# Kernel tuning notes

Hardware: AMD Instinct MI355X
Metric: run time of the kernel (lower is better)

Reference implementation:

```python
import jax, jax.numpy as jnp
import numpy as np

N_HIDDEN = 2048
N_HEADS = 64
EXPAND = 2
D_STATE = 128
D_CONV = 4
CHUNK = 128
DT_MIN = 0.001
DT_MAX = 0.1
INNER = EXPAND * N_HIDDEN            # 4096
HEAD_DIM = INNER // N_HEADS          # 64
CONV_DIM = INNER + 2 * D_STATE       # 4352
D_IN_PROJ = 2 * INNER + 2 * D_STATE + N_HEADS  # 8512
EPS = 1e-6


def setup_inputs() -> dict:
    key = jax.random.key(0)
    ks = jax.random.split(key, 10)
    B, L = 2, 2048
    s = lambda fan_in: 1.0 / np.sqrt(fan_in)
    return {
        "x": jax.random.normal(ks[0], (B, L, N_HIDDEN), jnp.float32),
        "W_in": jax.random.normal(ks[1], (N_HIDDEN, D_IN_PROJ), jnp.float32) * s(N_HIDDEN),
        "b_in": jnp.zeros((D_IN_PROJ,), jnp.float32),
        "conv_w": jax.random.normal(ks[2], (D_CONV, 1, CONV_DIM), jnp.float32) * s(D_CONV),
        "conv_b": jnp.zeros((CONV_DIM,), jnp.float32),
        "A_log": jnp.log(jnp.arange(1, N_HEADS + 1, dtype=jnp.float32)),
        "dt_bias": jax.random.normal(ks[3], (N_HEADS,), jnp.float32) * 0.1,
        "D_param": jnp.ones((N_HEADS,), jnp.float32),
        "norm_w": jnp.ones((INNER,), jnp.float32),
        "W_out": jax.random.normal(ks[4], (INNER, N_HIDDEN), jnp.float32) * s(INNER),
        "b_out": jnp.zeros((N_HIDDEN,), jnp.float32),
    }


def _segsum(x):
    t = x.shape[-1]
    cs = jnp.cumsum(x, axis=-1)
    seg = cs[..., :, None] - cs[..., None, :]
    mask = jnp.tril(jnp.ones((t, t), dtype=bool))
    return jnp.where(mask, seg, -jnp.inf)


def _ssd(x, dt, a, b_mat, c_mat, d, dt_bias):
    # x: (B,L,H,P)  dt: (B,L,H)  a: (H,)  b_mat/c_mat: (B,L,H,N)  d: (H,)
    bsz, seq, h, p = x.shape
    dt = jnp.clip(jax.nn.softplus(dt + dt_bias), DT_MIN, DT_MAX)
    d_res = d.reshape(1, 1, h, 1) * x
    x_disc = x * dt[..., None]
    a_disc = a * dt                                   # (B,L,H)
    ch = lambda t_: t_.reshape(bsz, seq // CHUNK, CHUNK, *t_.shape[2:])
    x_blk, b_blk, c_blk = ch(x_disc), ch(b_mat), ch(c_mat)
    a_blk = jnp.transpose(ch(a_disc), (0, 3, 1, 2))   # (B,H,C,Lc)
    a_cum = jnp.cumsum(a_blk, axis=-1)
    l_mat = jnp.exp(_segsum(a_blk))                   # (B,H,C,Lc,Lc)
    y_diag = jnp.einsum("bclhn,bcshn,bhcls,bcshp->bclhp", c_blk, b_blk, l_mat, x_blk)
    decay_states = jnp.exp(a_cum[..., -1:] - a_cum)
    states = jnp.einsum("bclhn,bhcl,bclhp->bchpn", b_blk, decay_states, x_blk)
    states = jnp.concatenate([jnp.zeros_like(states[:, :1]), states], axis=1)
    a_end = jnp.pad(a_cum[..., -1], ((0, 0), (0, 0), (1, 0)))
    decay_chunk = jnp.exp(_segsum(a_end))
    new_states = jnp.einsum("bhzc,bchpn->bzhpn", decay_chunk, states)
    states = new_states[:, :-1]
    y_off = jnp.einsum("bclhn,bchpn,bhcl->bclhp", c_blk, states, jnp.exp(a_cum))
    y = (y_diag + y_off).reshape(bsz, seq, h, p)
    return y + d_res


def reference(x, W_in, b_in, conv_w, conv_b, A_log, dt_bias, D_param, norm_w, W_out, b_out):
    B, L, _ = x.shape
    zxbcdt = x @ W_in + b_in
    z = zxbcdt[..., :INNER]
    xBC = zxbcdt[..., INNER:INNER + CONV_DIM]
    dt = zxbcdt[..., -N_HEADS:]
    # causal depthwise conv1d + silu
    xp = jnp.pad(xBC, ((0, 0), (D_CONV - 1, 0), (0, 0)))
    xBC = jax.lax.conv_general_dilated(
        xp, conv_w, window_strides=(1,), padding="VALID",
        dimension_numbers=("NWC", "WIO", "NWC"), feature_group_count=CONV_DIM,
    ) + conv_b
    xBC = jax.nn.silu(xBC)
    x_ssm = xBC[..., :INNER].reshape(B, L, N_HEADS, HEAD_DIM)
    b_mat = jnp.broadcast_to(xBC[..., INNER:INNER + D_STATE][:, :, None, :], (B, L, N_HEADS, D_STATE))
    c_mat = jnp.broadcast_to(xBC[..., INNER + D_STATE:][:, :, None, :], (B, L, N_HEADS, D_STATE))
    a = -jnp.exp(A_log)
    y = _ssd(x_ssm, dt, a, b_mat, c_mat, D_param, dt_bias)
    y = y.reshape(B, L, INNER)
    # gated RMSNorm
    y = y * jax.nn.silu(z)
    y = y * jax.lax.rsqrt(jnp.mean(y * y, axis=-1, keepdims=True) + EPS) * norm_w
    return y @ W_out + b_out
```

## Files before the change

kernel.cpp:

```cpp
#include <hip/hip_runtime.h>
#include <hip/hip_bf16.h>
#include <cstdint>

typedef __bf16 bf16x8 __attribute__((ext_vector_type(8)));
typedef __bf16 bf16x4 __attribute__((ext_vector_type(4)));
typedef float  f4     __attribute__((ext_vector_type(4)));

constexpr int BATCH   = 2;
constexpr int LSEQ    = 2048;
constexpr int NH      = 2048;
constexpr int INNER   = 4096;
constexpr int DSTATE  = 128;
constexpr int CONVD   = 4352;
constexpr int HEADS   = 64;
constexpr int HDIM    = 64;
constexpr int NPROJ   = 8512;
constexpr int NPROJ_P = 8576;
constexpr int NC      = 16;
constexpr int CH      = 128;
constexpr int ROWS    = BATCH * LSEQ;
constexpr int NBC     = BATCH * NC;

__device__ __forceinline__ f4 f4zero() { f4 v; v.x=0.f; v.y=0.f; v.z=0.f; v.w=0.f; return v; }

__device__ __forceinline__ void gload16(const __bf16* g, const char* l) {
    __builtin_amdgcn_global_load_lds((const __attribute__((address_space(1))) void*)g,
                                     (__attribute__((address_space(3))) void*)l, 16, 0, 0);
}

__global__ __launch_bounds__(256) void k_cast_bf16(const float* __restrict__ in,
                                                   __bf16* __restrict__ out, int n4) {
    int i = blockIdx.x * 256 + threadIdx.x;
    if (i >= n4) return;
    f4 v = ((const f4*)in)[i];
    bf16x4 o;
    o[0] = (__bf16)v.x; o[1] = (__bf16)v.y; o[2] = (__bf16)v.z; o[3] = (__bf16)v.w;
    ((bf16x4*)out)[i] = o;
}

__global__ __launch_bounds__(256) void k_transpose_cast(const float* __restrict__ in,
                                                        __bf16* __restrict__ out,
                                                        int R, int C, int Cp) {
    __shared__ float tile[32][33];
    int bn = blockIdx.x * 32, bk = blockIdx.y * 32;
    int tx = threadIdx.x & 31, ty = threadIdx.x >> 5;
#pragma unroll
    for (int i = 0; i < 4; ++i) {
        int k = bk + ty + i * 8, n = bn + tx;
        tile[ty + i * 8][tx] = (k < R && n < C) ? in[(size_t)k * C + n] : 0.f;
    }
    __syncthreads();
#pragma unroll
    for (int i = 0; i < 4; ++i) {
        int n = bn + ty + i * 8, k = bk + tx;
        if (n < Cp && k < R) out[(size_t)n * R + k] = (__bf16)tile[tx][ty + i * 8];
    }
}

template<int EPI>
__global__ __launch_bounds__(256, 2) void k_gemm128(
    const __bf16* __restrict__ A, const __bf16* __restrict__ Bt,
    const float* __restrict__ bias, float* __restrict__ Cf,
    __bf16* __restrict__ zf, __bf16* __restrict__ xbcpre, float* __restrict__ dtraw,
    int N, int K, int gridY) {
    extern __shared__ char smem[];
    constexpr int ABYTES = 128 * 128;
    constexpr int BUFB   = 2 * ABYTES;

    int tid = threadIdx.x, lane = tid & 63, w = tid >> 6;
    int wm = w >> 1, wn = w & 1;

    int bid = blockIdx.x;
    int q = gridDim.x >> 3;
    int wg = (bid & 7) * q + (bid >> 3);
    int bx = wg / gridY, by = wg - bx * gridY;
    int mBase = by * 128, nBase = bx * 128;

    int rl = lane & 15, rq = lane >> 4;
    int kslp = rq ^ (((rl >> 3) & 1) << 1);
    const int rdA = (wm * 64 + rl) * 64 + kslp * 16;
    const int rdB = ABYTES + (wn * 64 + rl) * 64 + kslp * 16;

    int lanep = lane ^ (((lane >> 5) & 1) << 1);
    int srs = lanep >> 2, sksl = lanep & 3;

    const __bf16* sA[4];
    const __bf16* sB[4];
#pragma unroll
    for (int li = 0; li < 4; ++li) {
        sA[li] = A  + (size_t)(mBase + (li & 1) * 64 + w * 16 + srs) * K + (li >> 1) * 32 + sksl * 8;
        sB[li] = Bt + (size_t)(nBase + (li & 1) * 64 + w * 16 + srs) * K + (li >> 1) * 32 + sksl * 8;
    }

    auto stageA = [&](int buf, int li, int kt) {
        gload16(sA[li] + kt, smem + buf * BUFB + (li >> 1) * 8192 + (li & 1) * 4096 + w * 1024);
    };
    auto stageB = [&](int buf, int li, int kt) {
        gload16(sB[li] + kt, smem + buf * BUFB + ABYTES + (li >> 1) * 8192 + (li & 1) * 4096 + w * 1024);
    };

    bf16x8 a0[4], b0[4], a1[4], b1[4];
    auto ldregs = [&](int bufoff, int ks, bf16x8* ar, bf16x8* br) {
#pragma unroll
        for (int i = 0; i < 4; ++i)
            ar[i] = *(const bf16x8*)(smem + bufoff + ks * 8192 + rdA + i * 1024);
#pragma unroll
        for (int i = 0; i < 4; ++i)
            br[i] = *(const bf16x8*)(smem + bufoff + ks * 8192 + rdB + i * 1024);
    };

    f4 acc[4][4];
#pragma unroll
    for (int i = 0; i < 4; ++i)
#pragma unroll
        for (int j = 0; j < 4; ++j) acc[i][j] = f4zero();

    auto domfma = [&](bf16x8* ar, bf16x8* br) {
        __builtin_amdgcn_s_setprio(1);
#pragma unroll
        for (int mi = 0; mi < 4; ++mi)
#pragma unroll
            for (int ni = 0; ni < 4; ++ni)
                acc[mi][ni] = __builtin_amdgcn_mfma_f32_16x16x32_bf16(ar[mi], br[ni], acc[mi][ni], 0, 0, 0);
        __builtin_amdgcn_s_setprio(0);
    };

    const int nt = K >> 6;
#pragma unroll
    for (int li = 0; li < 4; ++li) stageA(0, li, 0);
#pragma unroll
    for (int li = 0; li < 4; ++li) stageB(0, li, 0);
#pragma unroll
    for (int li = 0; li < 4; ++li) stageA(1, li, 64);
    asm volatile("s_waitcnt vmcnt(4)" ::: "memory");
    __builtin_amdgcn_s_barrier();
    ldregs(0, 0, a0, b0);

    for (int t = 0; t < nt; ++t) {
        const int cur = t & 1, bo = cur * BUFB;
        ldregs(bo, 1, a1, b1);
        if (t + 1 < nt) {
            const int ktn = (t + 1) << 6;
#pragma unroll
            for (int li = 0; li < 4; ++li) stageB(cur ^ 1, li, ktn);
        }
        __builtin_amdgcn_sched_barrier(0);
        domfma(a0, b0);
        asm volatile("s_waitcnt lgkmcnt(0)" ::: "memory");
        __builtin_amdgcn_sched_barrier(0);
        __builtin_amdgcn_s_barrier();
        if (t + 2 < nt) {
            const int ktn2 = (t + 2) << 6;
#pragma unroll
            for (int li = 0; li < 4; ++li) stageA(cur, li, ktn2);
        }
        __builtin_amdgcn_sched_barrier(0);
        domfma(a1, b1);
        if (t + 1 < nt) {
            if (t + 2 < nt) {
                asm volatile("s_waitcnt vmcnt(4)" ::: "memory");
            } else {
                asm volatile("s_waitcnt vmcnt(0)" ::: "memory");
            }
            __builtin_amdgcn_s_barrier();
            ldregs((cur ^ 1) * BUFB, 0, a0, b0);
        }
    }

    int cl = lane & 15, rq4 = (lane >> 4) * 4;
#pragma unroll
    for (int nf = 0; nf < 4; ++nf) {
        int col0 = nBase + wn * 64 + nf * 16;
        int col = col0 + cl;
        if constexpr (EPI == 1) {
            if (col0 >= NPROJ) continue;
            float bvv = bias[col];
#pragma unroll
            for (int mf = 0; mf < 4; ++mf) {
#pragma unroll
                for (int j = 0; j < 4; ++j) {
                    int row = mBase + wm * 64 + mf * 16 + rq4 + j;
                    float v = acc[mf][nf][j] + bvv;
                    if (col0 < INNER) {
                        zf[(size_t)row * INNER + col] = (__bf16)v;
                    } else if (col0 < INNER + CONVD) {
                        xbcpre[(size_t)row * CONVD + (col - INNER)] = (__bf16)v;
                    } else {
                        dtraw[(size_t)row * HEADS + (col - INNER - CONVD)] = v;
                    }
                }
            }
        } else {
            float bvv = bias[col];
#pragma unroll
            for (int mf = 0; mf < 4; ++mf)
#pragma unroll
                for (int j = 0; j < 4; ++j) {
                    int row = mBase + wm * 64 + mf * 16 + rq4 + j;
                    Cf[(size_t)row * N + col] = acc[mf][nf][j] + bvv;
                }
        }
    }
}

__global__ __launch_bounds__(256) void k_conv_silu(const __bf16* __restrict__ xbcpre,
                                                   const float* __restrict__ conv_w,
                                                   const float* __restrict__ conv_b,
                                                   __bf16* __restrict__ xbc) {
    int idx = blockIdx.x * 256 + threadIdx.x;
    int c8 = idx % (CONVD / 8);
    int bl = idx / (CONVD / 8);
    int l = bl & (LSEQ - 1);
    int c0 = c8 * 8;
    float acc[8];
    const f4* cb4 = (const f4*)(conv_b + c0);
    f4 b0 = cb4[0], b1 = cb4[1];
#pragma unroll
    for (int k = 0; k < 4; ++k) { acc[k] = b0[k]; acc[k + 4] = b1[k]; }
#pragma unroll
    for (int j = 0; j < 4; ++j) {
        int l2 = l + j - 3;
        if (l2 < 0) continue;
        bf16x8 xv = *(const bf16x8*)(xbcpre + (size_t)(bl + j - 3) * CONVD + c0);
        const f4* w4 = (const f4*)(conv_w + j * CONVD + c0);
        f4 w0 = w4[0], w1 = w4[1];
#pragma unroll
        for (int k = 0; k < 4; ++k) {
            acc[k]     += w0[k] * (float)xv[k];
            acc[k + 4] += w1[k] * (float)xv[k + 4];
        }
    }
    bf16x8 o;
#pragma unroll
    for (int k = 0; k < 8; ++k) {
        float a = acc[k];
        o[k] = (__bf16)(a / (1.f + expf(-a)));
    }
    *(bf16x8*)(xbc + (size_t)bl * CONVD + c0) = o;
}

__global__ __launch_bounds__(256) void k_dt(const float* __restrict__ dtraw,
                                            const float* __restrict__ dt_bias,
                                            float* __restrict__ dtp_t) {
    int idx = blockIdx.x * 256 + threadIdx.x;
    int h = idx & 63;
    int bl = idx >> 6;
    int b = bl >> 11, l = bl & (LSEQ - 1);
    float raw = dtraw[idx] + dt_bias[h];
    float sp = raw > 20.f ? raw : log1pf(expf(raw));
    dtp_t[((size_t)(b * HEADS + h)) * LSEQ + l] = fminf(fmaxf(sp, 0.001f), 0.1f);
}

__global__ __launch_bounds__(256) void k_transpose_bc(const __bf16* __restrict__ xbc,
                                                      __bf16* __restrict__ xT,
                                                      __bf16* __restrict__ BtG) {
    int bid = blockIdx.x;
    int ct = bid % 66;
    int rt = (bid / 66) & 1;
    int bc = bid / 132;
    __shared__ float T[64][65];
    int t = threadIdx.x;
    int lr0 = t >> 3, cg = t & 7;
#pragma unroll
    for (int it = 0; it < 2; ++it) {
        int lr = lr0 + it * 32;
        bf16x8 v = *(const bf16x8*)(xbc + (size_t)(bc * CH + rt * 64 + lr) * CONVD + ct * 64 + cg * 8);
#pragma unroll
        for (int j = 0; j < 8; ++j) T[lr][cg * 8 + j] = (float)v[j];
    }
    __syncthreads();
#pragma unroll
    for (int it = 0; it < 2; ++it) {
        int cl = lr0 + it * 32;
        int c = ct * 64 + cl;
        bf16x8 o;
#pragma unroll
        for (int j = 0; j < 8; ++j) o[j] = (__bf16)T[cg * 8 + j][cl];
        __bf16* dst = (c < INNER)
            ? xT  + ((size_t)bc * INNER + c) * CH + rt * 64 + cg * 8
            : BtG + ((size_t)bc * DSTATE + (c - INNER)) * CH + rt * 64 + cg * 8;
        *(bf16x8*)dst = o;
    }
}

__global__ __launch_bounds__(256) void k_cb(const __bf16* __restrict__ xbc,
                                            float* __restrict__ cbT) {
    int bid = blockIdx.x;
    int lg = bid & 7, bc = bid >> 3;
    int tid = threadIdx.x;
    int e0 = lg * 2048 + tid * 8;
    int l = e0 >> 7;
    int s0 = e0 & 127;
    const __bf16* Crow = xbc + (size_t)(bc * CH + l) * CONVD + INNER + DSTATE;
    const __bf16* B0   = xbc + (size_t)(bc * CH + s0) * CONVD + INNER;
    float acc[8];
#pragma unroll
    for (int j = 0; j < 8; ++j) acc[j] = 0.f;
    for (int n8 = 0; n8 < 16; ++n8) {
        bf16x8 cv = *(const bf16x8*)(Crow + n8 * 8);
        float cf[8];
#pragma unroll
        for (int k = 0; k < 8; ++k) cf[k] = (float)cv[k];
#pragma unroll
        for (int j = 0; j < 8; ++j) {
            bf16x8 bvv = *(const bf16x8*)(B0 + (size_t)j * CONVD + n8 * 8);
#pragma unroll
            for (int k = 0; k < 8; ++k) acc[j] += cf[k] * (float)bvv[k];
        }
    }
    float* dst = cbT + ((size_t)bc << 14) + (l << 7) + s0;
#pragma unroll
    for (int j = 0; j < 8; ++j) dst[j] = (s0 + j <= l) ? acc[j] : 0.f;
}

__global__ __launch_bounds__(256) void k_states(const __bf16* __restrict__ xT,
                                                const __bf16* __restrict__ BtG,
                                                const float* __restrict__ dtp_t,
                                                const float* __restrict__ A_log,
                                                __bf16* __restrict__ states,
                                                float* __restrict__ acum_buf,
                                                float* __restrict__ aend_buf) {
    int bid = blockIdx.x;
    int h = bid & 63, c = (bid >> 6) & 15, b = bid >> 10;
    int bc = b * NC + c, bh = b * HEADS + h;
    int tid = threadIdx.x;
    int lane = tid & 63, w = tid >> 6;
    __shared__ __bf16 Ab[64 * 136];
    __shared__ __bf16 Bb[128 * 136];
    __shared__ float s_ac[128], s_dt[128], s_e[128];
    float a_h = -expf(A_log[h]);

    if (tid < 128) {
        float d = dtp_t[(size_t)bh * LSEQ + c * CH + tid];
        s_dt[tid] = d;
        s_ac[tid] = a_h * d;
    }
    __syncthreads();
    for (int offd = 1; offd < 128; offd <<= 1) {
        float v = 0.f;
        if (tid < 128 && tid >= offd) v = s_ac[tid - offd];
        __syncthreads();
        if (tid < 128) s_ac[tid] += v;
        __syncthreads();
    }
    float aend = s_ac[127];
    if (tid < 128) {
        s_e[tid] = expf(aend - s_ac[tid]) * s_dt[tid];
        acum_buf[((size_t)bh * NC + c) * CH + tid] = s_ac[tid];
    }
    if (tid == 0) aend_buf[bh * NC + c] = aend;
    __syncthreads();

    const __bf16* xrow = xT + ((size_t)bc * INNER + h * HDIM) * CH;
#pragma unroll
    for (int it = 0; it < 4; ++it) {
        int task = it * 256 + tid;
        int p = task >> 4, lg2 = task & 15;
        bf16x8 v = *(const bf16x8*)(xrow + (size_t)p * CH + lg2 * 8);
        bf16x8 o;
#pragma unroll
        for (int j = 0; j < 8; ++j) o[j] = (__bf16)((float)v[j] * s_e[lg2 * 8 + j]);
        *(bf16x8*)&Ab[p * 136 + lg2 * 8] = o;
    }
    const __bf16* brow = BtG + (size_t)bc * DSTATE * CH;
#pragma unroll
    for (int it = 0; it < 8; ++it) {
        int task = it * 256 + tid;
        int n = task >> 4, lg2 = task & 15;
        *(bf16x8*)&Bb[n * 136 + lg2 * 8] = *(const bf16x8*)(brow + (size_t)n * CH + lg2 * 8);
    }
    __syncthreads();

    int rl = lane & 15, kq = (lane >> 4) * 8, rq = lane >> 4;
    f4 acc[8];
#pragma unroll
    for (int i = 0; i < 8; ++i) acc[i] = f4zero();
#pragma unroll
    for (int ks = 0; ks < 4; ++ks) {
        int k0 = ks * 32;
        bf16x8 a = *(const bf16x8*)&Ab[(w * 16 + rl) * 136 + k0 + kq];
#pragma unroll
        for (int nf = 0; nf < 8; ++nf) {
            bf16x8 bfr = *(const bf16x8*)&Bb[(nf * 16 + rl) * 136 + k0 + kq];
            acc[nf] = __builtin_amdgcn_mfma_f32_16x16x32_bf16(a, bfr, acc[nf], 0, 0, 0);
        }
    }
    __syncthreads();
#pragma unroll
    for (int nf = 0; nf < 8; ++nf)
#pragma unroll
        for (int j = 0; j < 4; ++j)
            Ab[(w * 16 + rq * 4 + j) * 136 + nf * 16 + rl] = (__bf16)acc[nf][j];
    __syncthreads();
    __bf16* sbase = states + ((size_t)(bc * HEADS + h)) * (HDIM * DSTATE);
#pragma unroll
    for (int it = 0; it < 4; ++it) {
        int task = it * 256 + tid;
        int p = task >> 4, ng = task & 15;
        *(bf16x8*)(sbase + (size_t)p * DSTATE + ng * 8) = *(const bf16x8*)&Ab[p * 136 + ng * 8];
    }
}

__global__ __launch_bounds__(128) void k_scan(__bf16* __restrict__ states,
                                              const float* __restrict__ aend_buf) {
    int s = blockIdx.x & 7;
    int bh = blockIdx.x >> 3;
    int b = bh >> 6, h = bh & 63;
    int tid = threadIdx.x;
    size_t off = (size_t)s * 1024 + (size_t)tid * 8;
    float run[8];
#pragma unroll
    for (int j = 0; j < 8; ++j) run[j] = 0.f;
    for (int c = 0; c < NC; ++c) {
        float dec = expf(aend_buf[bh * NC + c]);
        __bf16* base = states + ((size_t)((b * NC + c) * HEADS + h)) * (HDIM * DSTATE) + off;
        bf16x8 sv = *(bf16x8*)base;
        bf16x8 o;
#pragma unroll
        for (int j = 0; j < 8; ++j) o[j] = (__bf16)run[j];
        *(bf16x8*)base = o;
#pragma unroll
        for (int j = 0; j < 8; ++j) run[j] = run[j] * dec + (float)sv[j];
    }
}

__global__ __launch_bounds__(256) void k_out(const __bf16* __restrict__ xbc,
                                             const __bf16* __restrict__ xT,
                                             const float* __restrict__ dtp_t,
                                             const float* __restrict__ cbT,
                                             const __bf16* __restrict__ prev,
                                             const float* __restrict__ acum_buf,
                                             const float* __restrict__ D_param,
                                             __bf16* __restrict__ ybuf) {
    int bid = blockIdx.x;
    int h = bid & 63, c = (bid >> 6) & 15, b = bid >> 10;
    int bc = b * NC + c, bh = b * HEADS + h;
    int tid = threadIdx.x;
    int lane = tid & 63, w = tid >> 6;
    __shared__ __bf16 Ab[128 * 136];
    __shared__ __bf16 Bb[64 * 136];
    __shared__ float s_ac[128], s_dt[128];
    if (tid < 128) {
        s_ac[tid] = acum_buf[((size_t)bh * NC + c) * CH + tid];
        s_dt[tid] = dtp_t[(size_t)bh * LSEQ + c * CH + tid];
    }

#pragma unroll
    for (int it = 0; it < 8; ++it) {
        int task = it * 256 + tid;
        int l = task >> 4, ng = task & 15;
        *(bf16x8*)&Ab[l * 136 + ng * 8] =
            *(const bf16x8*)(xbc + (size_t)(bc * CH + l) * CONVD + INNER + DSTATE + ng * 8);
    }
    const __bf16* pbase = prev + ((size_t)(bc * HEADS + h)) * (HDIM * DSTATE);
#pragma unroll
    for (int it = 0; it < 4; ++it) {
        int task = it * 256 + tid;
        int p = task >> 4, ng = task & 15;
        *(bf16x8*)&Bb[p * 136 + ng * 8] = *(const bf16x8*)(pbase + (size_t)p * DSTATE + ng * 8);
    }
    __syncthreads();

    int rl = lane & 15, kq = (lane >> 4) * 8, rq = lane >> 4;
    f4 acc[2][4];
#pragma unroll
    for (int i = 0; i < 2; ++i)
#pragma unroll
        for (int j = 0; j < 4; ++j) acc[i][j] = f4zero();

#pragma unroll
    for (int ks = 0; ks < 4; ++ks) {
        int k0 = ks * 32;
        bf16x8 a0 = *(const bf16x8*)&Ab[(w * 32 + rl) * 136 + k0 + kq];
        bf16x8 a1 = *(const bf16x8*)&Ab[(w * 32 + 16 + rl) * 136 + k0 + kq];
#pragma unroll
        for (int nf = 0; nf < 4; ++nf) {
            bf16x8 bfr = *(const bf16x8*)&Bb[(nf * 16 + rl) * 136 + k0 + kq];
            acc[0][nf] = __builtin_amdgcn_mfma_f32_16x16x32_bf16(a0, bfr, acc[0][nf], 0, 0, 0);
            acc[1][nf] = __builtin_amdgcn_mfma_f32_16x16x32_bf16(a1, bfr, acc[1][nf], 0, 0, 0);
        }
    }
#pragma unroll
    for (int mf = 0; mf < 2; ++mf)
#pragma unroll
        for (int j = 0; j < 4; ++j) {
            float el = expf(s_ac[w * 32 + mf * 16 + rq * 4 + j]);
#pragma unroll
            for (int nf = 0; nf < 4; ++nf) acc[mf][nf][j] *= el;
        }
    __syncthreads();

    const float* cbb = cbT + ((size_t)bc << 14);
#pragma unroll
    for (int it = 0; it < 8; ++it) {
        int task = it * 256 + tid;
        int l = task >> 4, sg = task & 15;
        int s0 = sg * 8;
        const f4* cv4 = (const f4*)(cbb + (l << 7) + s0);
        f4 c0 = cv4[0], c1 = cv4[1];
        float acl = s_ac[l];
        bf16x8 o;
#pragma unroll
        for (int j = 0; j < 8; ++j) {
            int s = s0 + j;
            float cj = (j < 4) ? c0[j] : c1[j - 4];
            float m = 0.f;
            if (s <= l) m = cj * expf(acl - s_ac[s]) * s_dt[s];
            o[j] = (__bf16)m;
        }
        *(bf16x8*)&Ab[l * 136 + s0] = o;
    }
    const __bf16* xrow = xT + ((size_t)bc * INNER + h * HDIM) * CH;
#pragma unroll
    for (int it = 0; it < 4; ++it) {
        int task = it * 256 + tid;
        int p = task >> 4, lg2 = task & 15;
        *(bf16x8*)&Bb[p * 136 + lg2 * 8] = *(const bf16x8*)(xrow + (size_t)p * CH + lg2 * 8);
    }
    __syncthreads();

#pragma unroll
    for (int ks = 0; ks < 4; ++ks) {
        int k0 = ks * 32;
        bf16x8 a0 = *(const bf16x8*)&Ab[(w * 32 + rl) * 136 + k0 + kq];
        bf16x8 a1 = *(const bf16x8*)&Ab[(w * 32 + 16 + rl) * 136 + k0 + kq];
#pragma unroll
        for (int nf = 0; nf < 4; ++nf) {
            bf16x8 bfr = *(const bf16x8*)&Bb[(nf * 16 + rl) * 136 + k0 + kq];
            acc[0][nf] = __builtin_amdgcn_mfma_f32_16x16x32_bf16(a0, bfr, acc[0][nf], 0, 0, 0);
            acc[1][nf] = __builtin_amdgcn_mfma_f32_16x16x32_bf16(a1, bfr, acc[1][nf], 0, 0, 0);
        }
    }
    __syncthreads();

    float* yT = (float*)Ab;
#pragma unroll
    for (int mf = 0; mf < 2; ++mf)
#pragma unroll
        for (int nf = 0; nf < 4; ++nf)
#pragma unroll
            for (int j = 0; j < 4; ++j)
                yT[(w * 32 + mf * 16 + rq * 4 + j) * 68 + nf * 16 + rl] = acc[mf][nf][j];
    __syncthreads();

    float dh = D_param[h];
#pragma unroll
    for (int it = 0; it < 4; ++it) {
        int task = it * 256 + tid;
        int l = task >> 3, pg = task & 7;
        const f4* yv4 = (const f4*)&yT[l * 68 + pg * 8];
        f4 y0 = yv4[0], y1 = yv4[1];
        bf16x8 xv = *(const bf16x8*)(xbc + (size_t)(bc * CH + l) * CONVD + h * HDIM + pg * 8);
        bf16x8 o;
#pragma unroll
        for (int j = 0; j < 4; ++j) {
            o[j]     = (__bf16)(y0[j] + dh * (float)xv[j]);
            o[j + 4] = (__bf16)(y1[j] + dh * (float)xv[j + 4]);
        }
        *(bf16x8*)(ybuf + (size_t)(bc * CH + l) * INNER + h * HDIM + pg * 8) = o;
    }
}

__global__ __launch_bounds__(256) void k_gate_norm(__bf16* __restrict__ ybuf,
                                                   const __bf16* __restrict__ zf,
                                                   const float* __restrict__ norm_w) {
    int row = blockIdx.x, tid = threadIdx.x;
    bf16x8* yrow = (bf16x8*)(ybuf + (size_t)row * INNER);
    const bf16x8* zrow = (const bf16x8*)(zf + (size_t)row * INNER);
    float v[2][8];
    float ss = 0.f;
#pragma unroll
    for (int i = 0; i < 2; ++i) {
        bf16x8 yv = yrow[i * 256 + tid];
        bf16x8 zv = zrow[i * 256 + tid];
#pragma unroll
        for (int j = 0; j < 8; ++j) {
            float z = (float)zv[j];
            float t = (float)yv[j] * (z / (1.f + expf(-z)));
            v[i][j] = t;
            ss += t * t;
        }
    }
#pragma unroll
    for (int off = 32; off > 0; off >>= 1) ss += __shfl_down(ss, off, 64);
    __shared__ float red[4];
    __shared__ float scs;
    if ((tid & 63) == 0) red[tid >> 6] = ss;
    __syncthreads();
    if (tid == 0) scs = rsqrtf((red[0] + red[1] + red[2] + red[3]) * (1.f / INNER) + 1e-6f);
    __syncthreads();
    float scale = scs;
#pragma unroll
    for (int i = 0; i < 2; ++i) {
        const f4* nw = (const f4*)(norm_w + (i * 256 + tid) * 8);
        f4 w0 = nw[0], w1 = nw[1];
        bf16x8 o;
#pragma unroll
        for (int j = 0; j < 4; ++j) {
            o[j]     = (__bf16)(v[i][j]     * scale * w0[j]);
            o[j + 4] = (__bf16)(v[i][j + 4] * scale * w1[j]);
        }
        yrow[i * 256 + tid] = o;
    }
}

extern "C" void kernel_launch(void* const* d_in, const int* in_sizes, int n_in,
                              void* d_out, int out_size, void* d_ws, size_t ws_size,
                              hipStream_t stream) {
    const float* x       = (const float*)d_in[0];
    const float* W_in    = (const float*)d_in[1];
    const float* b_in    = (const float*)d_in[2];
    const float* conv_w  = (const float*)d_in[3];
    const float* conv_b  = (const float*)d_in[4];
    const float* A_log   = (const float*)d_in[5];
    const float* dt_bias = (const float*)d_in[6];
    const float* D_par   = (const float*)d_in[7];
    const float* norm_w  = (const float*)d_in[8];
    const float* W_out   = (const float*)d_in[9];
    const float* b_out   = (const float*)d_in[10];
    float* out = (float*)d_out;

    char* ws = (char*)d_ws;
    constexpr size_t SZ_XBF    = (size_t)ROWS * NH * 2;
    constexpr size_t SZ_WTIN   = (size_t)NPROJ_P * NH * 2;
    constexpr size_t SZ_R1     = SZ_XBF + SZ_WTIN;
    constexpr size_t SZ_ZF     = (size_t)ROWS * INNER * 2;
    constexpr size_t SZ_XBC    = (size_t)ROWS * CONVD * 2;
    constexpr size_t SZ_STATES = (size_t)NBC * HEADS * HDIM * DSTATE * 2;
    constexpr size_t SZ_CBT    = (size_t)NBC * CH * CH * 4;
    constexpr size_t SZ_ACUM   = (size_t)BATCH * HEADS * NC * CH * 4;
    constexpr size_t SZ_AEND   = (size_t)BATCH * HEADS * NC * 4;
    constexpr size_t SZ_DTP    = (size_t)ROWS * HEADS * 4;

    __bf16* xbf    = (__bf16*)(ws);
    __bf16* wtin   = (__bf16*)(ws + SZ_XBF);
    __bf16* zf     = (__bf16*)(ws + SZ_R1);
    __bf16* xbcpre = (__bf16*)(ws + SZ_R1 + SZ_ZF);
    __bf16* xbc    = (__bf16*)(ws + SZ_R1 + SZ_ZF + SZ_XBC);
    float*  dtraw  = (float*) (ws + SZ_R1 + SZ_ZF + 2 * SZ_XBC);
    __bf16* states = (__bf16*)(ws);
    float*  cbT    = (float*) (ws + SZ_STATES);
    float*  acum   = (float*) (ws + SZ_STATES + SZ_CBT);
    float*  aend   = (float*) (ws + SZ_STATES + SZ_CBT + SZ_ACUM);
    float*  dtp_t  = (float*) (ws + SZ_STATES + SZ_CBT + SZ_ACUM + SZ_AEND);
    __bf16* BtG    = (__bf16*)(ws + SZ_STATES + SZ_CBT + SZ_ACUM + SZ_AEND + SZ_DTP);
    __bf16* ybuf   = xbcpre;
    __bf16* wtout  = xbc;
    __bf16* xT     = (__bf16*)out;

    (void)ws_size; (void)in_sizes; (void)n_in; (void)out_size;

    hipFuncSetAttribute(reinterpret_cast<const void*>(&k_gemm128<1>),
                        hipFuncAttributeMaxDynamicSharedMemorySize, 65536);
    hipFuncSetAttribute(reinterpret_cast<const void*>(&k_gemm128<0>),
                        hipFuncAttributeMaxDynamicSharedMemorySize, 65536);

    k_cast_bf16<<<(ROWS * NH / 4 + 255) / 256, 256, 0, stream>>>(x, xbf, ROWS * NH / 4);
    k_transpose_cast<<<dim3(NPROJ_P / 32, NH / 32), 256, 0, stream>>>(W_in, wtin, NH, NPROJ, NPROJ_P);

    k_gemm128<1><<<(NPROJ_P / 128) * (ROWS / 128), 256, 65536, stream>>>(
        xbf, wtin, b_in, nullptr, zf, xbcpre, dtraw, NPROJ_P, NH, ROWS / 128);

    k_conv_silu<<<ROWS * (CONVD / 8) / 256, 256, 0, stream>>>(xbcpre, conv_w, conv_b, xbc);
    k_dt<<<ROWS * HEADS / 256, 256, 0, stream>>>(dtraw, dt_bias, dtp_t);
    k_transpose_bc<<<NBC * 132, 256, 0, stream>>>(xbc, xT, BtG);
    k_cb<<<NBC * 8, 256, 0, stream>>>(xbc, cbT);
    k_states<<<NBC * HEADS, 256, 0, stream>>>(xT, BtG, dtp_t, A_log, states, acum, aend);
    k_scan<<<BATCH * HEADS * 8, 128, 0, stream>>>(states, aend);
    k_out<<<NBC * HEADS, 256, 0, stream>>>(xbc, xT, dtp_t, cbT, states, acum, D_par, ybuf);
    k_gate_norm<<<ROWS, 256, 0, stream>>>(ybuf, zf, norm_w);

    k_transpose_cast<<<dim3(NH / 32, INNER / 32), 256, 0, stream>>>(W_out, wtout, INNER, NH, NH);
    k_gemm128<0><<<(NH / 128) * (ROWS / 128), 256, 65536, stream>>>(
        ybuf, wtout, b_out, out, nullptr, nullptr, nullptr, NH, INNER, ROWS / 128);
}
```

Baseline: 488.8 us.

## Replace output projection GEMM with 8-wave 256x128 pipelined kernel

Adds a new templated GEMM kernel with 512 threads (8 waves), 256x128 tiles, double-buffered LDS with split staging interleaved between two MFMA half-steps, wave priority boosting, and XCD-aware block remapping. It is used only for the output projection (4096x2048x4096), replacing the 128x128 256-thread kernel. The aim is to hide global-load latency behind MFMA work and raise per-block compute density, at the cost of more LDS (96KB) and fewer resident blocks.

```diff
diff --git a/kernel.cpp b/kernel.cpp
--- a/kernel.cpp
+++ b/kernel.cpp
@@ -200,6 +200,133 @@
                     Cf[(size_t)row * N + col] = acc[mf][nf][j] + bvv;
                 }
         }
+    }
+}
+
+template<int BM, int BN, int WM, int WN>
+__global__ __launch_bounds__(512, 2) void k_gemm8(
+    const __bf16* __restrict__ A, const __bf16* __restrict__ Bt,
+    const float* __restrict__ bias, float* __restrict__ Cf,
+    int N, int K, int gridY) {
+    extern __shared__ char smem[];
+    constexpr int MFRAG = BM / (WM * 16);
+    constexpr int NFRAG = BN / (WN * 16);
+    constexpr int ALINES = BM / 64, BLINES = BN / 64, LT = ALINES + BLINES;
+    constexpr int ABYTES = BM * 128, BUFB = ABYTES + BN * 128;
+    constexpr int LPPA = BM / 128, LPPB = BN / 128;
+
+    int tid = threadIdx.x, lane = tid & 63, w = tid >> 6;
+    int wm = w / WN, wn = w % WN;
+
+    int bid = blockIdx.x;
+    int q = gridDim.x >> 3;
+    int wg = (bid & 7) * q + (bid >> 3);
+    int bx = wg / gridY, by = wg - bx * gridY;
+    int mBase = by * BM, nBase = bx * BN;
+
+    int rl = lane & 15, rq = lane >> 4;
+    int kslp = rq ^ (((rl >> 3) & 1) << 1);
+    const int rdA = (wm * MFRAG * 16 + rl) * 64 + kslp * 16;
+    const int rdB = ABYTES + (wn * NFRAG * 16 + rl) * 64 + kslp * 16;
+
+    int lanep = lane ^ (((lane >> 5) & 1) << 1);
+    int srs = lanep >> 2, sksl = lanep & 3;
+
+    const __bf16* sA[ALINES];
+#pragma unroll
+    for (int li = 0; li < ALINES; ++li)
+        sA[li] = A + (size_t)(mBase + (li % LPPA) * 128 + w * 16 + srs) * K + (li / LPPA) * 32 + sksl * 8;
+    const __bf16* sB[BLINES];
+#pragma unroll
+    for (int li = 0; li < BLINES; ++li)
+        sB[li] = Bt + (size_t)(nBase + (li % LPPB) * 128 + w * 16 + srs) * K + (li / LPPB) * 32 + sksl * 8;
+
+    auto stage = [&](int buf, int line, int kt) {
+        if (line < ALINES) {
+            gload16(sA[line] + kt, smem + buf * BUFB + line * 8192 + w * 1024);
+        } else {
+            int lb = line - ALINES;
+            gload16(sB[lb] + kt, smem + buf * BUFB + ABYTES + lb * 8192 + w * 1024);
+        }
+    };
+
+    bf16x8 a0[MFRAG], b0[NFRAG], a1[MFRAG], b1[NFRAG];
+    auto ldregs = [&](int bufoff, int ks, bf16x8* ar, bf16x8* br) {
+#pragma unroll
+        for (int i = 0; i < MFRAG; ++i)
+            ar[i] = *(const bf16x8*)(smem + bufoff + ks * (BM * 64) + rdA + i * 1024);
+#pragma unroll
+        for (int i = 0; i < NFRAG; ++i)
+            br[i] = *(const bf16x8*)(smem + bufoff + ks * (BN * 64) + rdB + i * 1024);
+    };
+
+    f4 acc[MFRAG][NFRAG];
+#pragma unroll
+    for (int i = 0; i < MFRAG; ++i)
+#pragma unroll
+        for (int j = 0; j < NFRAG; ++j) acc[i][j] = f4zero();
+
+    auto domfma = [&](bf16x8* ar, bf16x8* br) {
+        __builtin_amdgcn_s_setprio(1);
+#pragma unroll
+        for (int mi = 0; mi < MFRAG; ++mi)
+#pragma unroll
+            for (int ni = 0; ni < NFRAG; ++ni)
+                acc[mi][ni] = __builtin_amdgcn_mfma_f32_16x16x32_bf16(ar[mi], br[ni], acc[mi][ni], 0, 0, 0);
+        __builtin_amdgcn_s_setprio(0);
+    };
+
+    const int nt = K >> 6;
+#pragma unroll
+    for (int li = 0; li < LT; ++li) stage(0, li, 0);
+#pragma unroll
+    for (int li = 0; li < 4; ++li) stage(1, li, 64);
+    asm volatile("s_waitcnt vmcnt(4)" ::: "memory");
+    __builtin_amdgcn_s_barrier();
+    ldregs(0, 0, a0, b0);
+
+    for (int t = 0; t < nt; ++t) {
+        const int cur = t & 1;
+        const int bufoff = cur * BUFB;
+        ldregs(bufoff, 1, a1, b1);
+        if (t + 1 < nt) {
+#pragma unroll
+            for (int li = 4; li < LT; ++li) stage(cur ^ 1, li, (t + 1) << 6);
+        }
+        __builtin_amdgcn_sched_barrier(0);
+        domfma(a0, b0);
+        asm volatile("s_waitcnt lgkmcnt(0)" ::: "memory");
+        __builtin_amdgcn_sched_barrier(0);
+        __builtin_amdgcn_s_barrier();
+        if (t + 2 < nt) {
+#pragma unroll
+            for (int li = 0; li < 4; ++li) stage(cur, li, (t + 2) << 6);
+        }
+        __builtin_amdgcn_sched_barrier(0);
+        domfma(a1, b1);
+        if (t + 1 < nt) {
+            if (t + 2 < nt) {
+                asm volatile("s_waitcnt vmcnt(4)" ::: "memory");
+            } else {
+                asm volatile("s_waitcnt vmcnt(0)" ::: "memory");
+            }
+            __builtin_amdgcn_s_barrier();
+            ldregs((cur ^ 1) * BUFB, 0, a0, b0);
+        }
+    }
+
+    int cl = lane & 15, rq4 = (lane >> 4) * 4;
+#pragma unroll
+    for (int nf = 0; nf < NFRAG; ++nf) {
+        int col = nBase + wn * NFRAG * 16 + nf * 16 + cl;
+        float bvv = bias[col];
+#pragma unroll
+        for (int mf = 0; mf < MFRAG; ++mf)
+#pragma unroll
+            for (int j = 0; j < 4; ++j) {
+                int row = mBase + wm * MFRAG * 16 + mf * 16 + rq4 + j;
+                Cf[(size_t)row * N + col] = acc[mf][nf][j] + bvv;
+            }
     }
 }
 
@@ -652,8 +779,8 @@
 
     hipFuncSetAttribute(reinterpret_cast<const void*>(&k_gemm128<1>),
                         hipFuncAttributeMaxDynamicSharedMemorySize, 65536);
-    hipFuncSetAttribute(reinterpret_cast<const void*>(&k_gemm128<0>),
-                        hipFuncAttributeMaxDynamicSharedMemorySize, 65536);
+    hipFuncSetAttribute(reinterpret_cast<const void*>(&k_gemm8<256,128,4,2>),
+                        hipFuncAttributeMaxDynamicSharedMemorySize, 98304);
 
     k_cast_bf16<<<(ROWS * NH / 4 + 255) / 256, 256, 0, stream>>>(x, xbf, ROWS * NH / 4);
     k_transpose_cast<<<dim3(NPROJ_P / 32, NH / 32), 256, 0, stream>>>(W_in, wtin, NH, NPROJ, NPROJ_P);
@@ -671,6 +798,6 @@
     k_gate_norm<<<ROWS, 256, 0, stream>>>(ybuf, zf, norm_w);
 
     k_transpose_cast<<<dim3(NH / 32, INNER / 32), 256, 0, stream>>>(W_out, wtout, INNER, NH, NH);
-    k_gemm128<0><<<(NH / 128) * (ROWS / 128), 256, 65536, stream>>>(
-        ybuf, wtout, b_out, out, nullptr, nullptr, nullptr, NH, INNER, ROWS / 128);
-}
+    k_gemm8<256,128,4,2><<<(NH / 128) * (ROWS / 256), 512, 98304, stream>>>(
+        ybuf, wtout, b_out, out, NH, INNER, ROWS / 256);
+}
```

After: 481.0 us. About the same (-1.6%).
